# Kernel tuning notes

Hardware: AMD Instinct MI355X
Metric: run time of the kernel (lower is better)

The kernel has to match this reference:

```python
import jax, jax.numpy as jnp
import numpy as np

EMB = 1024
HEADS = 16


def setup_inputs() -> dict:
    key = jax.random.key(0)
    k1, k2, k3, k4, k5 = jax.random.split(key, 5)
    b, n = 2, 2048
    x = jax.random.normal(k1, (b, n, EMB), dtype=jnp.float32)
    Wqkv = jax.random.normal(k2, (EMB, 3 * EMB), dtype=jnp.float32) * (EMB ** -0.5)
    bqkv = jax.random.normal(k3, (3 * EMB,), dtype=jnp.float32) * 0.02
    Wproj = jax.random.normal(k4, (EMB, EMB), dtype=jnp.float32) * (EMB ** -0.5)
    bproj = jax.random.normal(k5, (EMB,), dtype=jnp.float32) * 0.02
    return {"x": x, "Wqkv": Wqkv, "bqkv": bqkv, "Wproj": Wproj, "bproj": bproj}


def reference(x, Wqkv, bqkv, Wproj, bproj):
    b, n, e = x.shape
    h = HEADS
    d = e // h
    qkv = x @ Wqkv + bqkv                      # [b, n, 3e]
    # rearrange 'b n (h d qkv) -> qkv b h n d' : qkv index is innermost
    qkv = qkv.reshape(b, n, h, d, 3)
    qkv = jnp.transpose(qkv, (4, 0, 2, 1, 3))  # [3, b, h, n, d]
    q, k, v = qkv[0], qkv[1], qkv[2]
    energy = jnp.einsum('bhqd,bhkd->bhqk', q, k)
    scaling = jnp.float32(e) ** 0.5            # NOTE: sqrt(emb_size), not head_dim
    att = jax.nn.softmax(energy / scaling, axis=-1)
    out = jnp.einsum('bhql,bhld->bhqd', att, v)
    out = jnp.transpose(out, (0, 2, 1, 3)).reshape(b, n, e)  # 'b h n d -> b n (h d)'
    return out @ Wproj + bproj
```

## Files before the change

### kernel.cpp

```cpp
#include <hip/hip_runtime.h>
#include <hip/hip_bf16.h>
#include <stdint.h>

typedef __bf16 bf16;
typedef __attribute__((ext_vector_type(8))) __bf16 bf16x8;
typedef __attribute__((ext_vector_type(4))) __bf16 bf16x4;
typedef __attribute__((ext_vector_type(4))) float f32x4;
typedef __attribute__((ext_vector_type(16))) float f32x16;

#define MFMA16(a, b, c) __builtin_amdgcn_mfma_f32_16x16x32_bf16((a), (b), (c), 0, 0, 0)
#define MFMA32(a, b, c) __builtin_amdgcn_mfma_f32_32x32x16_bf16((a), (b), (c), 0, 0, 0)

#define QSCALE 0.045084220027780106f

__device__ __forceinline__ void glds16(const void* g, void* l) {
  __builtin_amdgcn_global_load_lds(
      (const __attribute__((address_space(1))) void*)g,
      (__attribute__((address_space(3))) void*)l, 16, 0, 0);
}

__device__ __forceinline__ bf16x8 ldsfrag(const unsigned char* base, int row, int colb) {
  return *(const bf16x8*)(base + row * 128 + (colb ^ ((row & 7) << 4)));
}

__device__ __forceinline__ uint32_t pkbf16(float a, float b) {
  uint32_t r;
  asm("v_cvt_pk_bf16_f32 %0, %1, %2" : "=v"(r) : "v"(a), "v"(b));
  return r;
}

__device__ __forceinline__ float fexp2(float x) {
#if __has_builtin(__builtin_amdgcn_exp2f)
  return __builtin_amdgcn_exp2f(x);
#else
  float r;
  asm("v_exp_f32 %0, %1" : "=v"(r) : "v"(x));
  return r;
#endif
}

__device__ __forceinline__ f32x16 zero16() {
  f32x16 v;
#pragma unroll
  for (int i = 0; i < 16; ++i) v[i] = 0.f;
  return v;
}

__global__ __launch_bounds__(256) void k_prep_x(const float* __restrict__ x, bf16* __restrict__ xb) {
  int gid = blockIdx.x * 256 + threadIdx.x;
  const f32x4* xv = (const f32x4*)x;
  f32x4 a = xv[(size_t)gid * 2], b = xv[(size_t)gid * 2 + 1];
  bf16x8 o;
#pragma unroll
  for (int i = 0; i < 4; ++i) { o[i] = (bf16)a[i]; o[i + 4] = (bf16)b[i]; }
  *(bf16x8*)(xb + (size_t)gid * 8) = o;
}

template <int MODE>
__global__ __launch_bounds__(256) void k_prep_w(const float* __restrict__ W, bf16* __restrict__ WT) {
  __shared__ float tile[64][256];
  const int C = (MODE == 0) ? 3072 : 1024;
  const int c0 = blockIdx.x * 256, k0 = blockIdx.y * 64;
  const int lw = threadIdx.x & 63, w = threadIdx.x >> 6;
#pragma unroll
  for (int i = 0; i < 16; ++i) {
    int r = i * 4 + w;
    f32x4 v = *(const f32x4*)(W + (size_t)(k0 + r) * C + c0 + lw * 4);
    *(f32x4*)&tile[r][lw * 4] = v;
  }
  __syncthreads();
  const int c = c0 + threadIdx.x;
  int j;
  float sc = 1.0f;
  if (MODE == 0) {
    int h = c / 192, rem = c - h * 192, dd = rem / 3, wh = rem - dd * 3;
    j = wh * 1024 + h * 64 + dd;
    if (wh == 0) sc = QSCALE;
  } else {
    j = c;
  }
#pragma unroll
  for (int ch = 0; ch < 8; ++ch) {
    bf16x8 o;
#pragma unroll
    for (int i = 0; i < 8; ++i) o[i] = (bf16)(tile[ch * 8 + i][threadIdx.x] * sc);
    *(bf16x8*)(WT + (size_t)j * 1024 + k0 + ch * 8) = o;
  }
}

__global__ __launch_bounds__(256) void k_prep_bias(const float* __restrict__ bqkv, float* __restrict__ bp) {
  int gid = blockIdx.x * 256 + threadIdx.x;
  int wj = gid >> 10, rr = gid & 1023, hh = rr >> 6, d2 = rr & 63;
  float v = bqkv[hh * 192 + d2 * 3 + wj];
  bp[gid] = (wj == 0) ? v * QSCALE : v;
}

template <int EPI>
__global__ __launch_bounds__(256) void k_gemm(const bf16* __restrict__ A, const bf16* __restrict__ BT,
                                              const float* __restrict__ bias, bf16* __restrict__ qk,
                                              bf16* __restrict__ vt, float* __restrict__ outf) {
  __shared__ __align__(16) unsigned char sA[16384];
  __shared__ __align__(16) unsigned char sB[16384];
  const int tid = threadIdx.x;
  const int l = tid & 63, w = tid >> 6, g = l >> 4, l15 = l & 15;
  const int wr = w >> 1, wc = w & 1;
  const int bm = blockIdx.y, bn = blockIdx.x;
  const unsigned char* Ab = (const unsigned char*)A + (size_t)bm * 128 * 2048;
  const unsigned char* Bb = (const unsigned char*)BT + (size_t)bn * 128 * 2048;
  f32x4 acc[4][4];
#pragma unroll
  for (int mi = 0; mi < 4; ++mi)
#pragma unroll
    for (int ni = 0; ni < 4; ++ni) acc[mi][ni] = (f32x4){0.f, 0.f, 0.f, 0.f};

  for (int kt = 0; kt < 16; ++kt) {
    const int k0b = kt * 128;
#pragma unroll
    for (int p = 0; p < 4; ++p) {
      int co = (p * 256 + tid) * 16;
      int row = co >> 7, wb = co & 127;
      int sw = wb ^ ((row & 7) << 4);
      glds16(Ab + (size_t)row * 2048 + k0b + sw, sA + co);
      glds16(Bb + (size_t)row * 2048 + k0b + sw, sB + co);
    }
    __syncthreads();
#pragma unroll
    for (int ks = 0; ks < 2; ++ks) {
      bf16x8 af[4], bfr[4];
#pragma unroll
      for (int mi = 0; mi < 4; ++mi) af[mi] = ldsfrag(sA, wr * 64 + mi * 16 + l15, ks * 64 + g * 16);
#pragma unroll
      for (int ni = 0; ni < 4; ++ni) bfr[ni] = ldsfrag(sB, wc * 64 + ni * 16 + l15, ks * 64 + g * 16);
      __builtin_amdgcn_s_setprio(1);
#pragma unroll
      for (int mi = 0; mi < 4; ++mi)
#pragma unroll
        for (int ni = 0; ni < 4; ++ni) acc[mi][ni] = MFMA16(af[mi], bfr[ni], acc[mi][ni]);
      __builtin_amdgcn_s_setprio(0);
    }
    __syncthreads();
  }
#pragma unroll
  for (int ni = 0; ni < 4; ++ni) {
    int j = bn * 128 + wc * 64 + ni * 16 + l15;
    float bj = bias[j];
#pragma unroll
    for (int mi = 0; mi < 4; ++mi) {
      int m0 = bm * 128 + wr * 64 + mi * 16 + g * 4;
      float v[4];
#pragma unroll
      for (int rr = 0; rr < 4; ++rr) v[rr] = acc[mi][ni][rr] + bj;
      if (EPI == 0) {
        int which = j >> 10, r = j & 1023, h = r >> 6, dd = r & 63;
        int b = m0 >> 11, nn = m0 & 2047;
        if (which < 2) {
#pragma unroll
          for (int rr = 0; rr < 4; ++rr)
            qk[(size_t)which * 4194304 + (((size_t)b * 16 + h) * 2048 + nn + rr) * 64 + dd] = (bf16)v[rr];
        } else {
          bf16x4 pw = {(bf16)v[0], (bf16)v[1], (bf16)v[2], (bf16)v[3]};
          *(bf16x4*)(vt + (((size_t)b * 16 + h) * 64 + dd) * 2048 + nn) = pw;
        }
      } else {
#pragma unroll
        for (int rr = 0; rr < 4; ++rr) outf[(size_t)(m0 + rr) * 1024 + j] = v[rr];
      }
    }
  }
}

__global__ __launch_bounds__(512, 2) void k_attn(const bf16* __restrict__ Qg, const bf16* __restrict__ Kg,
                                                 const bf16* __restrict__ VTg, bf16* __restrict__ Og) {
  __shared__ __align__(16) unsigned char smem[66560];
  const int tid = threadIdx.x;
  const int l = tid & 63, w = tid >> 6;
  const int q = l & 31, hi = l >> 5;
  const int g = w >> 2, wl = w & 3;
  const int stid = tid & 255;

  const int bid = blockIdx.x;
  const int wg = (bid & 7) * 64 + (bid >> 3);
  const int bh = wg >> 4;
  const int q0w = (wg & 15) * 128 + wl * 32;

  bf16x8 qf[4];
#pragma unroll
  for (int ks = 0; ks < 4; ++ks)
    qf[ks] = *(const bf16x8*)(Qg + ((size_t)bh * 2048 + q0w + q) * 64 + ks * 16 + hi * 8);

  f32x16 oacc[2];
  oacc[0] = zero16();
  oacc[1] = zero16();
  float lrun4[4] = {0.f, 0.f, 0.f, 0.f};
  bf16x8 pb[4];

  const unsigned char* Kb = (const unsigned char*)Kg + (size_t)bh * 262144 + (size_t)g * 131072;
  const unsigned char* Vb = (const unsigned char*)VTg + (size_t)bh * 262144 + (size_t)g * 2048;
  unsigned char* sKg = smem + g * 16384;
  unsigned char* sVg = smem + 32768 + g * 16384;

  const int co0 = stid * 16, co1 = (256 + stid) * 16;
  const int row0 = co0 >> 7, row1 = co1 >> 7;
  const int sw0 = (co0 & 127) ^ ((row0 & 7) << 4), sw1 = (co1 & 127) ^ ((row1 & 7) << 4);

#define STAGE_K(kb_, buf_)                                                        \
  do {                                                                            \
    const unsigned char* Ksrc = Kb + (size_t)(kb_) * 8192;                        \
    glds16(Ksrc + (co0 & ~127) + sw0, sKg + (buf_) * 8192 + co0);                 \
    glds16(Ksrc + (co1 & ~127) + sw1, sKg + (buf_) * 8192 + co1);                 \
  } while (0)
#define STAGE_V(kb_, buf_)                                                        \
  do {                                                                            \
    glds16(Vb + (size_t)row0 * 4096 + (size_t)(kb_) * 128 + sw0, sVg + (buf_) * 8192 + co0); \
    glds16(Vb + (size_t)row1 * 4096 + (size_t)(kb_) * 128 + sw1, sVg + (buf_) * 8192 + co1); \
  } while (0)

#define QK_EXP_PACK(kbase_)                                                       \
  do {                                                                            \
    _Pragma("unroll") for (int kt = 0; kt < 2; ++kt) {                            \
      f32x16 sacc = zero16();                                                     \
      __builtin_amdgcn_s_setprio(1);                                              \
      _Pragma("unroll") for (int ks = 0; ks < 4; ++ks) {                          \
        bf16x8 kf = ldsfrag((kbase_), kt * 32 + q, ks * 32 + hi * 16);            \
        sacc = MFMA32(kf, qf[ks], sacc);                                          \
      }                                                                           \
      __builtin_amdgcn_s_setprio(0);                                              \
      float pe[16];                                                               \
      _Pragma("unroll") for (int r = 0; r < 16; ++r) pe[r] = fexp2(sacc[r]);      \
      _Pragma("unroll") for (int m = 0; m < 4; ++m)                               \
        _Pragma("unroll") for (int j = 0; j < 4; ++j) lrun4[j] += pe[4 * m + j];  \
      uint32_t c[4][2];                                                           \
      _Pragma("unroll") for (int m = 0; m < 4; ++m) {                             \
        c[m][0] = pkbf16(pe[4 * m], pe[4 * m + 1]);                               \
        c[m][1] = pkbf16(pe[4 * m + 2], pe[4 * m + 3]);                           \
      }                                                                           \
      _Pragma("unroll") for (int s = 0; s < 2; ++s) {                             \
        uint32_t x0 = c[2 * s][0], y0 = c[2 * s + 1][0];                          \
        uint32_t x1 = c[2 * s][1], y1 = c[2 * s + 1][1];                          \
        asm("v_permlane32_swap_b32 %0, %1" : "+v"(x0), "+v"(y0));                 \
        asm("v_permlane32_swap_b32 %0, %1" : "+v"(x1), "+v"(y1));                 \
        union { uint32_t u[4]; bf16x8 v; } bfr;                                   \
        bfr.u[0] = x0; bfr.u[1] = x1; bfr.u[2] = y0; bfr.u[3] = y1;               \
        pb[kt * 2 + s] = bfr.v;                                                   \
      }                                                                           \
    }                                                                             \
  } while (0)

#define PV_TILE(vbase_)                                                           \
  do {                                                                            \
    __builtin_amdgcn_s_setprio(1);                                                \
    _Pragma("unroll") for (int ks = 0; ks < 4; ++ks)                              \
      _Pragma("unroll") for (int dt = 0; dt < 2; ++dt) {                          \
        bf16x8 vf = ldsfrag((vbase_), dt * 32 + q, ks * 32 + hi * 16);            \
        oacc[dt] = MFMA32(vf, pb[ks], oacc[dt]);                                  \
      }                                                                           \
    __builtin_amdgcn_s_setprio(0);                                                \
  } while (0)

  STAGE_K(0, 0);
  STAGE_V(0, 0);
  __syncthreads();
  STAGE_K(1, 1);
  QK_EXP_PACK(sKg);
  __syncthreads();
  int cur = 0;

  for (int kb = 0; kb < 15; ++kb) {
    const int nxt = cur ^ 1;
    if (kb < 14) STAGE_K(kb + 2, cur);
    STAGE_V(kb + 1, nxt);
    PV_TILE(sVg + cur * 8192);
    QK_EXP_PACK(sKg + nxt * 8192);
    __syncthreads();
    cur = nxt;
  }
  PV_TILE(sVg + cur * 8192);

#undef STAGE_K
#undef STAGE_V
#undef QK_EXP_PACK
#undef PV_TILE

  float lrun = (lrun4[0] + lrun4[1]) + (lrun4[2] + lrun4[3]);

  float* mbuf = (float*)smem;
  float* lb = (float*)(smem + 65536);
  if (g == 1) {
#pragma unroll
    for (int dt = 0; dt < 2; ++dt)
#pragma unroll
      for (int r = 0; r < 16; ++r) mbuf[((wl * 32 + dt * 16 + r) << 6) + l] = oacc[dt][r];
    lb[wl * 64 + l] = lrun;
  }
  __syncthreads();
  if (g == 0) {
#pragma unroll
    for (int dt = 0; dt < 2; ++dt)
#pragma unroll
      for (int r = 0; r < 16; ++r) oacc[dt][r] += mbuf[((wl * 32 + dt * 16 + r) << 6) + l];
    float lr = lrun + lb[wl * 64 + l];
    float ps = lr + __shfl_xor(lr, 32);
    float linv = 1.0f / ps;
    unsigned char* sO = smem + 32768 + wl * 4096;
#pragma unroll
    for (int dt = 0; dt < 2; ++dt)
#pragma unroll
      for (int m = 0; m < 4; ++m) {
        uint32_t b0 = pkbf16(oacc[dt][4 * m] * linv, oacc[dt][4 * m + 1] * linv);
        uint32_t b1 = pkbf16(oacc[dt][4 * m + 2] * linv, oacc[dt][4 * m + 3] * linv);
        int byteo = (dt * 64 + m * 16 + hi * 8) ^ ((q & 7) << 4);
        uint32_t* dst = (uint32_t*)(sO + q * 128 + byteo);
        dst[0] = b0; dst[1] = b1;
      }
    const int b = bh >> 4, h = bh & 15;
#pragma unroll
    for (int rd = 0; rd < 4; ++rd) {
      int byteo = hi * 64 + rd * 16;
      bf16x8 v = *(const bf16x8*)(sO + q * 128 + (byteo ^ ((q & 7) << 4)));
      *(bf16x8*)(Og + ((size_t)b * 2048 + q0w + q) * 1024 + h * 64 + byteo / 2) = v;
    }
  }
}

extern "C" void kernel_launch(void* const* d_in, const int* in_sizes, int n_in,
                              void* d_out, int out_size, void* d_ws, size_t ws_size,
                              hipStream_t stream) {
  const float* x = (const float*)d_in[0];
  const float* Wqkv = (const float*)d_in[1];
  const float* bqkv = (const float*)d_in[2];
  const float* Wproj = (const float*)d_in[3];
  const float* bproj = (const float*)d_in[4];
  float* out = (float*)d_out;
  char* ws = (char*)d_ws;

  bf16* XB = (bf16*)(ws + 0);
  bf16* WQT = (bf16*)(ws + 8388608);
  float* BQP = (float*)(ws + 14680064);
  bf16* WPT = (bf16*)(ws + 14696448);
  bf16* Q = (bf16*)(ws + 16793600);
  bf16* K = (bf16*)(ws + 25182208);
  bf16* VT = (bf16*)(ws + 33570816);
  bf16* AO = XB;
  (void)K;
  (void)ws_size;

  k_prep_x<<<2048, 256, 0, stream>>>(x, XB);
  k_prep_w<0><<<dim3(12, 16), 256, 0, stream>>>(Wqkv, WQT);
  k_prep_w<1><<<dim3(4, 16), 256, 0, stream>>>(Wproj, WPT);
  k_prep_bias<<<12, 256, 0, stream>>>(bqkv, BQP);
  k_gemm<0><<<dim3(24, 32), 256, 0, stream>>>(XB, WQT, BQP, Q, VT, nullptr);
  k_attn<<<512, 512, 0, stream>>>(Q, Q + 4194304, VT, AO);
  k_gemm<1><<<dim3(8, 32), 256, 0, stream>>>(AO, WPT, bproj, nullptr, nullptr, out);
}
```

Baseline: 128.8 us.

## Process two query tiles per wave in attention to reuse K/V fragments

Result: faster. 123.6 us (-4.0%).

```diff
diff --git a/kernel.cpp b/kernel.cpp
--- a/kernel.cpp
+++ b/kernel.cpp
@@ -169,9 +169,9 @@
   }
 }
 
-__global__ __launch_bounds__(512, 2) void k_attn(const bf16* __restrict__ Qg, const bf16* __restrict__ Kg,
+__global__ __launch_bounds__(512, 1) void k_attn(const bf16* __restrict__ Qg, const bf16* __restrict__ Kg,
                                                  const bf16* __restrict__ VTg, bf16* __restrict__ Og) {
-  __shared__ __align__(16) unsigned char smem[66560];
+  __shared__ __align__(16) unsigned char smem[67584];
   const int tid = threadIdx.x;
   const int l = tid & 63, w = tid >> 6;
   const int q = l & 31, hi = l >> 5;
@@ -179,20 +179,22 @@
   const int stid = tid & 255;
 
   const int bid = blockIdx.x;
-  const int wg = (bid & 7) * 64 + (bid >> 3);
-  const int bh = wg >> 4;
-  const int q0w = (wg & 15) * 128 + wl * 32;
-
-  bf16x8 qf[4];
-#pragma unroll
-  for (int ks = 0; ks < 4; ++ks)
-    qf[ks] = *(const bf16x8*)(Qg + ((size_t)bh * 2048 + q0w + q) * 64 + ks * 16 + hi * 8);
-
-  f32x16 oacc[2];
-  oacc[0] = zero16();
-  oacc[1] = zero16();
-  float lrun4[4] = {0.f, 0.f, 0.f, 0.f};
-  bf16x8 pb[4];
+  const int wg = (bid & 7) * 32 + (bid >> 3);
+  const int bh = wg >> 3;
+  const int q0w = (wg & 7) * 256 + wl * 64;
+
+  bf16x8 qf[2][4];
+#pragma unroll
+  for (int qt = 0; qt < 2; ++qt)
+#pragma unroll
+    for (int ks = 0; ks < 4; ++ks)
+      qf[qt][ks] = *(const bf16x8*)(Qg + ((size_t)bh * 2048 + q0w + qt * 32 + q) * 64 + ks * 16 + hi * 8);
+
+  f32x16 oacc[2][2];
+#pragma unroll
+  for (int qt = 0; qt < 2; ++qt) { oacc[qt][0] = zero16(); oacc[qt][1] = zero16(); }
+  float lrun4[2][4] = {{0.f, 0.f, 0.f, 0.f}, {0.f, 0.f, 0.f, 0.f}};
+  bf16x8 pb[2][4];
 
   const unsigned char* Kb = (const unsigned char*)Kg + (size_t)bh * 262144 + (size_t)g * 131072;
   const unsigned char* Vb = (const unsigned char*)VTg + (size_t)bh * 262144 + (size_t)g * 2048;
@@ -218,30 +220,33 @@
 #define QK_EXP_PACK(kbase_)                                                       \
   do {                                                                            \
     _Pragma("unroll") for (int kt = 0; kt < 2; ++kt) {                            \
-      f32x16 sacc = zero16();                                                     \
-      __builtin_amdgcn_s_setprio(1);                                              \
-      _Pragma("unroll") for (int ks = 0; ks < 4; ++ks) {                          \
-        bf16x8 kf = ldsfrag((kbase_), kt * 32 + q, ks * 32 + hi * 16);            \
-        sacc = MFMA32(kf, qf[ks], sacc);                                          \
-      }                                                                           \
-      __builtin_amdgcn_s_setprio(0);                                              \
-      float pe[16];                                                               \
-      _Pragma("unroll") for (int r = 0; r < 16; ++r) pe[r] = fexp2(sacc[r]);      \
-      _Pragma("unroll") for (int m = 0; m < 4; ++m)                               \
-        _Pragma("unroll") for (int j = 0; j < 4; ++j) lrun4[j] += pe[4 * m + j];  \
-      uint32_t c[4][2];                                                           \
-      _Pragma("unroll") for (int m = 0; m < 4; ++m) {                             \
-        c[m][0] = pkbf16(pe[4 * m], pe[4 * m + 1]);                               \
-        c[m][1] = pkbf16(pe[4 * m + 2], pe[4 * m + 3]);                           \
-      }                                                                           \
-      _Pragma("unroll") for (int s = 0; s < 2; ++s) {                             \
-        uint32_t x0 = c[2 * s][0], y0 = c[2 * s + 1][0];                          \
-        uint32_t x1 = c[2 * s][1], y1 = c[2 * s + 1][1];                          \
-        asm("v_permlane32_swap_b32 %0, %1" : "+v"(x0), "+v"(y0));                 \
-        asm("v_permlane32_swap_b32 %0, %1" : "+v"(x1), "+v"(y1));                 \
-        union { uint32_t u[4]; bf16x8 v; } bfr;                                   \
-        bfr.u[0] = x0; bfr.u[1] = x1; bfr.u[2] = y0; bfr.u[3] = y1;               \
-        pb[kt * 2 + s] = bfr.v;                                                   \
+      bf16x8 kf[4];                                                               \
+      _Pragma("unroll") for (int ks = 0; ks < 4; ++ks)                            \
+        kf[ks] = ldsfrag((kbase_), kt * 32 + q, ks * 32 + hi * 16);               \
+      _Pragma("unroll") for (int qt = 0; qt < 2; ++qt) {                          \
+        f32x16 sacc = zero16();                                                   \
+        __builtin_amdgcn_s_setprio(1);                                            \
+        _Pragma("unroll") for (int ks = 0; ks < 4; ++ks)                          \
+          sacc = MFMA32(kf[ks], qf[qt][ks], sacc);                                \
+        __builtin_amdgcn_s_setprio(0);                                            \
+        float pe[16];                                                             \
+        _Pragma("unroll") for (int r = 0; r < 16; ++r) pe[r] = fexp2(sacc[r]);    \
+        _Pragma("unroll") for (int m = 0; m < 4; ++m)                             \
+          _Pragma("unroll") for (int j = 0; j < 4; ++j) lrun4[qt][j] += pe[4 * m + j]; \
+        uint32_t c[4][2];                                                         \
+        _Pragma("unroll") for (int m = 0; m < 4; ++m) {                           \
+          c[m][0] = pkbf16(pe[4 * m], pe[4 * m + 1]);                             \
+          c[m][1] = pkbf16(pe[4 * m + 2], pe[4 * m + 3]);                         \
+        }                                                                         \
+        _Pragma("unroll") for (int s = 0; s < 2; ++s) {                           \
+          uint32_t x0 = c[2 * s][0], y0 = c[2 * s + 1][0];                        \
+          uint32_t x1 = c[2 * s][1], y1 = c[2 * s + 1][1];                        \
+          asm("v_permlane32_swap_b32 %0, %1" : "+v"(x0), "+v"(y0));               \
+          asm("v_permlane32_swap_b32 %0, %1" : "+v"(x1), "+v"(y1));               \
+          union { uint32_t u[4]; bf16x8 v; } bfr;                                 \
+          bfr.u[0] = x0; bfr.u[1] = x1; bfr.u[2] = y0; bfr.u[3] = y1;             \
+          pb[qt][kt * 2 + s] = bfr.v;                                             \
+        }                                                                         \
       }                                                                           \
     }                                                                             \
   } while (0)
@@ -252,7 +257,8 @@
     _Pragma("unroll") for (int ks = 0; ks < 4; ++ks)                              \
       _Pragma("unroll") for (int dt = 0; dt < 2; ++dt) {                          \
         bf16x8 vf = ldsfrag((vbase_), dt * 32 + q, ks * 32 + hi * 16);            \
-        oacc[dt] = MFMA32(vf, pb[ks], oacc[dt]);                                  \
+        _Pragma("unroll") for (int qt = 0; qt < 2; ++qt)                          \
+          oacc[qt][dt] = MFMA32(vf, pb[qt][ks], oacc[qt][dt]);                    \
       }                                                                           \
     __builtin_amdgcn_s_setprio(0);                                                \
   } while (0)
@@ -281,43 +287,60 @@
 #undef QK_EXP_PACK
 #undef PV_TILE
 
-  float lrun = (lrun4[0] + lrun4[1]) + (lrun4[2] + lrun4[3]);
+  float lrun[2];
+#pragma unroll
+  for (int qt = 0; qt < 2; ++qt)
+    lrun[qt] = (lrun4[qt][0] + lrun4[qt][1]) + (lrun4[qt][2] + lrun4[qt][3]);
 
   float* mbuf = (float*)smem;
   float* lb = (float*)(smem + 65536);
   if (g == 1) {
 #pragma unroll
-    for (int dt = 0; dt < 2; ++dt)
-#pragma unroll
-      for (int r = 0; r < 16; ++r) mbuf[((wl * 32 + dt * 16 + r) << 6) + l] = oacc[dt][r];
-    lb[wl * 64 + l] = lrun;
+    for (int qt = 0; qt < 2; ++qt) {
+#pragma unroll
+      for (int dt = 0; dt < 2; ++dt)
+#pragma unroll
+        for (int r = 0; r < 16; ++r)
+          mbuf[((wl * 64 + qt * 32 + dt * 16 + r) << 6) + l] = oacc[qt][dt][r];
+      lb[(wl * 2 + qt) * 64 + l] = lrun[qt];
+    }
   }
   __syncthreads();
   if (g == 0) {
 #pragma unroll
-    for (int dt = 0; dt < 2; ++dt)
-#pragma unroll
-      for (int r = 0; r < 16; ++r) oacc[dt][r] += mbuf[((wl * 32 + dt * 16 + r) << 6) + l];
-    float lr = lrun + lb[wl * 64 + l];
-    float ps = lr + __shfl_xor(lr, 32);
-    float linv = 1.0f / ps;
+    for (int qt = 0; qt < 2; ++qt)
+#pragma unroll
+      for (int dt = 0; dt < 2; ++dt)
+#pragma unroll
+        for (int r = 0; r < 16; ++r)
+          oacc[qt][dt][r] += mbuf[((wl * 64 + qt * 32 + dt * 16 + r) << 6) + l];
+  }
+  __syncthreads();
+  if (g == 0) {
+    const int b = bh >> 4, h = bh & 15;
     unsigned char* sO = smem + 32768 + wl * 4096;
 #pragma unroll
-    for (int dt = 0; dt < 2; ++dt)
-#pragma unroll
-      for (int m = 0; m < 4; ++m) {
-        uint32_t b0 = pkbf16(oacc[dt][4 * m] * linv, oacc[dt][4 * m + 1] * linv);
-        uint32_t b1 = pkbf16(oacc[dt][4 * m + 2] * linv, oacc[dt][4 * m + 3] * linv);
-        int byteo = (dt * 64 + m * 16 + hi * 8) ^ ((q & 7) << 4);
-        uint32_t* dst = (uint32_t*)(sO + q * 128 + byteo);
-        dst[0] = b0; dst[1] = b1;
+    for (int qt = 0; qt < 2; ++qt) {
+      float lr = lrun[qt] + lb[(wl * 2 + qt) * 64 + l];
+      float ps = lr + __shfl_xor(lr, 32);
+      float linv = 1.0f / ps;
+#pragma unroll
+      for (int dt = 0; dt < 2; ++dt)
+#pragma unroll
+        for (int m = 0; m < 4; ++m) {
+          uint32_t b0 = pkbf16(oacc[qt][dt][4 * m] * linv, oacc[qt][dt][4 * m + 1] * linv);
+          uint32_t b1 = pkbf16(oacc[qt][dt][4 * m + 2] * linv, oacc[qt][dt][4 * m + 3] * linv);
+          int byteo = (dt * 64 + m * 16 + hi * 8) ^ ((q & 7) << 4);
+          uint32_t* dst = (uint32_t*)(sO + q * 128 + byteo);
+          dst[0] = b0; dst[1] = b1;
+        }
+      const int q0 = q0w + qt * 32;
+#pragma unroll
+      for (int rd = 0; rd < 4; ++rd) {
+        int byteo = hi * 64 + rd * 16;
+        bf16x8 v = *(const bf16x8*)(sO + q * 128 + (byteo ^ ((q & 7) << 4)));
+        *(bf16x8*)(Og + ((size_t)b * 2048 + q0 + q) * 1024 + h * 64 + byteo / 2) = v;
       }
-    const int b = bh >> 4, h = bh & 15;
-#pragma unroll
-    for (int rd = 0; rd < 4; ++rd) {
-      int byteo = hi * 64 + rd * 16;
-      bf16x8 v = *(const bf16x8*)(sO + q * 128 + (byteo ^ ((q & 7) << 4)));
-      *(bf16x8*)(Og + ((size_t)b * 2048 + q0w + q) * 1024 + h * 64 + byteo / 2) = v;
     }
   }
 }
@@ -349,6 +372,6 @@
   k_prep_w<1><<<dim3(4, 16), 256, 0, stream>>>(Wproj, WPT);
   k_prep_bias<<<12, 256, 0, stream>>>(bqkv, BQP);
   k_gemm<0><<<dim3(24, 32), 256, 0, stream>>>(XB, WQT, BQP, Q, VT, nullptr);
-  k_attn<<<512, 512, 0, stream>>>(Q, Q + 4194304, VT, AO);
+  k_attn<<<256, 512, 0, stream>>>(Q, Q + 4194304, VT, AO);
   k_gemm<1><<<dim3(8, 32), 256, 0, stream>>>(AO, WPT, bproj, nullptr, nullptr, out);
 }
```
